# Optimization experiments

Hardware: AMD Instinct MI355X
Metric: run time of the kernel (lower is better)

## Reference

```python
import jax, jax.numpy as jnp
import numpy as np

EPS = 1e-8
TAU = 0.2
IOU_THR = 0.5
NEG = -1e9
N, C, H, D_FG, D_CLS = 8192, 1024, 256, 64, 128


def setup_inputs() -> dict:
    key = jax.random.key(0)
    ks = jax.random.split(key, 11)
    def lin(k, fan_in, fan_out):
        return jax.random.normal(k, (fan_in, fan_out), jnp.float32) / np.sqrt(fan_in)
    return {
        "roi_feats": jax.random.normal(ks[0], (N, C), jnp.float32),
        "labels": jax.random.randint(ks[1], (N,), 0, 21, jnp.int32).astype(jnp.int64),
        "ious": jax.random.uniform(ks[2], (N,), jnp.float32),
        "fg_w1": lin(ks[3], C, H), "fg_b1": jnp.zeros((H,), jnp.float32),
        "fg_w2": lin(ks[4], H, D_FG), "fg_b2": jnp.zeros((D_FG,), jnp.float32),
        "cls_w1": lin(ks[5], C, H), "cls_b1": jnp.zeros((H,), jnp.float32),
        "cls_w2": lin(ks[6], H, D_CLS), "cls_b2": jnp.zeros((D_CLS,), jnp.float32),
    }


def _project_normalize(x, w1, b1, w2, b2):
    h = jax.nn.relu(x @ w1 + b1)
    z = h @ w2 + b2
    norm = jnp.maximum(jnp.linalg.norm(z, axis=1, keepdims=True), EPS)
    return z / norm


def _forward(roi_feats, labels, ious, fg_w1, fg_b1, fg_w2, fg_b2, cls_w1, cls_b1, cls_w2, cls_b2):
    n = roi_feats.shape[0]
    z_fg = _project_normalize(roi_feats, fg_w1, fg_b1, fg_w2, fg_b2)
    z_cls = _project_normalize(roi_feats, cls_w1, cls_b1, cls_w2, cls_b2)

    ignore = labels == -1
    fg = (labels > 0) & ~ignore
    iou_weight = jnp.where(ious > IOU_THR, ious, 0.0)
    eye = jnp.eye(n, dtype=bool)

    # ---- fg/bg contrastive (bg_as_negatives_only=True) ----
    sim_fg = (z_fg @ z_fg.T) / TAU                       # [N,N]
    exp_sim = jnp.exp(sim_fg)
    denom = jnp.sum(exp_sim * (~eye).astype(jnp.float32), axis=1)
    pos = (fg & ~ignore)[None, :] & ~eye                 # positives: fg columns, no self
    n_pos = jnp.sum(pos, axis=1)
    numer = jnp.sum(exp_sim * pos.astype(jnp.float32), axis=1)
    # original computes den = denom + EPS then -log((numer+EPS)/(den+EPS))
    loss_i = -jnp.log((numer + EPS) / (denom + 2.0 * EPS))
    valid = (fg & ~ignore) & (n_pos > 0)
    w = iou_weight * valid.astype(jnp.float32)
    loss_fg_bg = jnp.sum(w * loss_i) / (jnp.sum(w) + EPS)

    # ---- class supervised contrastive ----
    sim_cls = (z_cls @ z_cls.T) / TAU
    sim_masked = jnp.where(eye, NEG, sim_cls)
    log_denom = jax.nn.logsumexp(sim_masked, axis=1)     # [N]
    log_p = jnp.where(eye, NEG, sim_cls - log_denom[:, None])
    # pos_mask keeps diagonal (as in original): same label, col not ignore, col label != 0
    posc = (labels[None, :] == labels[:, None]) & (~ignore)[None, :] & (labels[None, :] != 0)
    n_posc = jnp.sum(posc, axis=1).astype(jnp.float32)
    sum_log_p = jnp.sum(log_p * posc.astype(jnp.float32), axis=1)
    valid_c = (fg & ~ignore) & (n_posc > 0) & jnp.isfinite(log_denom)
    Lzi = jnp.where(valid_c, -sum_log_p / (n_posc + EPS), 0.0)
    wc = iou_weight * valid_c.astype(jnp.float32)
    loss_supcon = jnp.sum(wc * Lzi) / (jnp.sum(wc) + EPS)

    return jnp.stack([loss_fg_bg, loss_supcon])


def reference(roi_feats, labels, ious, fg_w1, fg_b1, fg_w2, fg_b2, cls_w1, cls_b1, cls_w2, cls_b2):
    return _forward(roi_feats, labels, ious, fg_w1, fg_b1, fg_w2, fg_b2, cls_w1, cls_b1, cls_w2, cls_b2)
```

## Files before the change

kernel.cpp:

```cpp
#include <hip/hip_runtime.h>


typedef __attribute__((ext_vector_type(8))) short bs8;
typedef __attribute__((ext_vector_type(4))) float f4;

#define MFMA_BF16(a, b, c) __builtin_amdgcn_mfma_f32_16x16x32_bf16((a), (b), (c), 0, 0, 0)

#if defined(__has_builtin)
#if __has_builtin(__builtin_amdgcn_exp2f)
#define EXP2F(x) __builtin_amdgcn_exp2f(x)
#endif
#endif
#ifndef EXP2F
__device__ __forceinline__ float __exp2_raw(float x) {
  float r;
  asm volatile("v_exp_f32 %0, %1" : "=v"(r) : "v"(x));
  return r;
}
#define EXP2F(x) __exp2_raw(x)
#endif

#define SQRT_KL2E 2.6857914f
#define LN2F      0.6931471805599453f

__device__ __forceinline__ unsigned short f2bf(float f) {
  unsigned int u = __float_as_uint(f);
  u = (u + 0x7fffu + ((u >> 16) & 1u)) >> 16;
  return (unsigned short)u;
}
__device__ __forceinline__ float bf2f(unsigned short s) {
  return __uint_as_float(((unsigned int)s) << 16);
}
__device__ __forceinline__ unsigned int pk_trunc(float a, float b) {
  return __builtin_amdgcn_perm(__float_as_uint(b), __float_as_uint(a), 0x07060302u);
}

constexpr size_t O_W1T  = 0;
constexpr size_t O_W2TF = 1048576;
constexpr size_t O_W2TC = 1081344;
constexpr size_t O_SCLS = 1146880;
constexpr size_t O_ROWD = 1163264;
constexpr size_t O_ROWN = 1196032;
constexpr size_t O_ROWS = 1228800;
constexpr size_t O_SCAL = 1261568;
constexpr size_t O_HIST = 1261584;
constexpr size_t O_NFG  = 1261712;
constexpr size_t O_H    = 1261824;
constexpr size_t O_ZF   = 9650432;
constexpr size_t O_ZC   = 10699008;
constexpr size_t O_XB   = 12796160;
constexpr size_t WS_NEED_XB = O_XB + 16777216;
constexpr int ZERO_WORDS = (int)((O_SCAL + 16 - O_SCLS) / 4);

__global__ void __launch_bounds__(256) prep_kernel(
    const float* __restrict__ X, const int* __restrict__ labels,
    const float* __restrict__ fgw1, const float* __restrict__ clsw1,
    const float* __restrict__ fgw2, const float* __restrict__ clsw2,
    unsigned short* __restrict__ W1T, unsigned short* __restrict__ W2Tf,
    unsigned short* __restrict__ W2Tc, float* __restrict__ zerop,
    int* __restrict__ hist, int* __restrict__ nfg,
    unsigned short* __restrict__ Xb) {
  const int bx = blockIdx.x, t = threadIdx.x;
  if (bx < 113) {
    int i = bx * 256 + t;
    if (i < ZERO_WORDS) zerop[i] = 0.f;
    return;
  }
  if (bx == 113) {
    __shared__ int sh[33];
    if (t < 33) sh[t] = 0;
    __syncthreads();
    for (int it = 0; it < 32; it++) {
      int lab = labels[it * 256 + t];
      if (lab >= 0 && lab < 32) atomicAdd(&sh[lab], 1);
      if (lab > 0) atomicAdd(&sh[32], 1);
    }
    __syncthreads();
    if (t < 32) hist[t] = sh[t];
    if (t == 32) *nfg = sh[32];
    return;
  }
  if (bx < 254) {
    __shared__ float tile[64][65];
    int lb = bx - 114;
    const float* src; unsigned short* dst; int R, C, lt;
    if (lb < 64)       { src = fgw1;  dst = W1T;              R = 1024; C = 256; lt = lb; }
    else if (lb < 128) { src = clsw1; dst = W1T + 256 * 1024; R = 1024; C = 256; lt = lb - 64; }
    else if (lb < 132) { src = fgw2;  dst = W2Tf;             R = 256;  C = 64;  lt = lb - 128; }
    else               { src = clsw2; dst = W2Tc;             R = 256;  C = 128; lt = lb - 132; }
    const int cT = C >> 6;
    const int r0 = (lt / cT) << 6, c0 = (lt % cT) << 6;
    {
      const int rr = t >> 4, cc = (t & 15) << 2;
#pragma unroll
      for (int i = 0; i < 4; i++) {
        float4 v = *(const float4*)(src + (size_t)(r0 + rr + i * 16) * C + c0 + cc);
        tile[rr + i * 16][cc] = v.x; tile[rr + i * 16][cc + 1] = v.y;
        tile[rr + i * 16][cc + 2] = v.z; tile[rr + i * 16][cc + 3] = v.w;
      }
    }
    __syncthreads();
    {
      const int dr = t >> 2, dc = (t & 3) << 4;
      bs8 o0, o1;
#pragma unroll
      for (int j = 0; j < 8; j++) o0[j] = (short)f2bf(tile[dc + j][dr]);
#pragma unroll
      for (int j = 0; j < 8; j++) o1[j] = (short)f2bf(tile[dc + 8 + j][dr]);
      unsigned short* dp = dst + (size_t)(c0 + dr) * R + r0 + dc;
      *(bs8*)dp = o0;
      *(bs8*)(dp + 8) = o1;
    }
    return;
  }
  {
    int i = (bx - 254) * 2048 + t * 8;
    float4 x0 = *(const float4*)(X + i);
    float4 x1 = *(const float4*)(X + i + 4);
    uint4 pk;
    pk.x = pk_trunc(x0.x, x0.y);
    pk.y = pk_trunc(x0.z, x0.w);
    pk.z = pk_trunc(x1.x, x1.y);
    pk.w = pk_trunc(x1.z, x1.w);
    *(uint4*)(Xb + i) = pk;
  }
}

__global__ void __launch_bounds__(256) gemm1x_kernel(
    const unsigned short* __restrict__ Xb, const unsigned short* __restrict__ W1T,
    const float* __restrict__ b1f, const float* __restrict__ b1c,
    unsigned short* __restrict__ H) {
  __shared__ __align__(16) unsigned short lA[128 * 72];
  __shared__ __align__(16) unsigned short lB[64 * 72];
  const int t = threadIdx.x;
  const int w = t >> 6, lane = t & 63, ln = lane & 15, quad = lane >> 4;
  const int m0 = blockIdx.x * 128, n0 = blockIdx.y * 64;

  f4 acc[2][4];
#pragma unroll
  for (int rs = 0; rs < 2; rs++)
#pragma unroll
    for (int s = 0; s < 4; s++) acc[rs][s] = (f4){0.f, 0.f, 0.f, 0.f};

  for (int k0 = 0; k0 < 1024; k0 += 64) {
    __syncthreads();
#pragma unroll
    for (int i = 0; i < 4; i++) {
      int c = i * 256 + t, r = c >> 3, ke = (c & 7) * 8;
      *(bs8*)&lA[r * 72 + ke] = *(const bs8*)(Xb + (size_t)(m0 + r) * 1024 + k0 + ke);
    }
#pragma unroll
    for (int i = 0; i < 2; i++) {
      int c = i * 256 + t, r = c >> 3, ke = (c & 7) * 8;
      *(bs8*)&lB[r * 72 + ke] = *(const bs8*)(W1T + (size_t)(n0 + r) * 1024 + k0 + ke);
    }
    __syncthreads();
#pragma unroll
    for (int kk = 0; kk < 2; kk++) {
      bs8 a0 = *(const bs8*)&lA[(w * 32 + ln) * 72 + kk * 32 + quad * 8];
      bs8 a1 = *(const bs8*)&lA[(w * 32 + 16 + ln) * 72 + kk * 32 + quad * 8];
#pragma unroll
      for (int s = 0; s < 4; s++) {
        bs8 bf = *(const bs8*)&lB[(s * 16 + ln) * 72 + kk * 32 + quad * 8];
        acc[0][s] = MFMA_BF16(a0, bf, acc[0][s]);
        acc[1][s] = MFMA_BF16(a1, bf, acc[1][s]);
      }
    }
  }
#pragma unroll
  for (int s = 0; s < 4; s++) {
    int n = n0 + s * 16 + ln;
    float b = (n < 256) ? b1f[n] : b1c[n - 256];
#pragma unroll
    for (int rs = 0; rs < 2; rs++)
#pragma unroll
      for (int r = 0; r < 4; r++) {
        float v = fmaxf(acc[rs][s][r] + b, 0.f);
        H[(size_t)(m0 + w * 32 + rs * 16 + quad * 4 + r) * 512 + n] = f2bf(v);
      }
  }
}

__global__ void __launch_bounds__(256) gemm1f_kernel(
    const float* __restrict__ X, const unsigned short* __restrict__ W1T,
    const float* __restrict__ b1f, const float* __restrict__ b1c,
    unsigned short* __restrict__ H) {
  __shared__ __align__(16) unsigned short lA[128 * 40];
  __shared__ __align__(16) unsigned short lB[64 * 40];
  const int t = threadIdx.x;
  const int w = t >> 6, lane = t & 63, ln = lane & 15, quad = lane >> 4;
  const int m0 = blockIdx.x * 128, n0 = blockIdx.y * 64;
  f4 acc[2][4];
#pragma unroll
  for (int rs = 0; rs < 2; rs++)
#pragma unroll
    for (int s = 0; s < 4; s++) acc[rs][s] = (f4){0.f, 0.f, 0.f, 0.f};
  for (int k0 = 0; k0 < 1024; k0 += 32) {
    __syncthreads();
#pragma unroll
    for (int i = 0; i < 2; i++) {
      int ch = t + i * 256;
      int r = ch >> 2, c = (ch & 3) * 8;
      const float* xp = X + (size_t)(m0 + r) * 1024 + k0 + c;
      float4 x0 = *(const float4*)xp;
      float4 x1 = *(const float4*)(xp + 4);
      uint4 pk;
      pk.x = pk_trunc(x0.x, x0.y); pk.y = pk_trunc(x0.z, x0.w);
      pk.z = pk_trunc(x1.x, x1.y); pk.w = pk_trunc(x1.z, x1.w);
      *(uint4*)&lA[r * 40 + c] = pk;
    }
    {
      int r = t >> 2, c = (t & 3) * 8;
      *(bs8*)&lB[r * 40 + c] = *(const bs8*)(W1T + (size_t)(n0 + r) * 1024 + k0 + c);
    }
    __syncthreads();
    bs8 af0 = *(const bs8*)&lA[(w * 32 + ln) * 40 + quad * 8];
    bs8 af1 = *(const bs8*)&lA[(w * 32 + 16 + ln) * 40 + quad * 8];
#pragma unroll
    for (int s = 0; s < 4; s++) {
      bs8 bf = *(const bs8*)&lB[(s * 16 + ln) * 40 + quad * 8];
      acc[0][s] = MFMA_BF16(af0, bf, acc[0][s]);
      acc[1][s] = MFMA_BF16(af1, bf, acc[1][s]);
    }
  }
#pragma unroll
  for (int s = 0; s < 4; s++) {
    int n = n0 + s * 16 + ln;
    float b = (n < 256) ? b1f[n] : b1c[n - 256];
#pragma unroll
    for (int rs = 0; rs < 2; rs++)
#pragma unroll
      for (int r = 0; r < 4; r++) {
        float v = fmaxf(acc[rs][s][r] + b, 0.f);
        H[(size_t)(m0 + w * 32 + rs * 16 + quad * 4 + r) * 512 + n] = f2bf(v);
      }
  }
}

__global__ void __launch_bounds__(256) gemm2_kernel(
    const unsigned short* __restrict__ H,
    const unsigned short* __restrict__ W2Tf, const unsigned short* __restrict__ W2Tc,
    const float* __restrict__ b2f, const float* __restrict__ b2c,
    unsigned short* __restrict__ Zf, unsigned short* __restrict__ Zc) {
  __shared__ float lredf[64][17];
  __shared__ float lredc[64][33];
  const int t = threadIdx.x;
  const int w = t >> 6, lane = t & 63, ln = lane & 15, quad = lane >> 4;
  const int rw = blockIdx.x * 16;
  const int kh = w & 1;

  if (w < 2) {
    const unsigned short* hrow = H + (size_t)(rw + ln) * 512 + kh * 128;
    f4 acc[4];
#pragma unroll
    for (int s = 0; s < 4; s++) acc[s] = (f4){0.f, 0.f, 0.f, 0.f};
#pragma unroll
    for (int ks = 0; ks < 4; ks++) {
      bs8 af = *(const bs8*)(hrow + ks * 32 + quad * 8);
#pragma unroll
      for (int s = 0; s < 4; s++) {
        bs8 bf = *(const bs8*)(W2Tf + (size_t)(s * 16 + ln) * 256 + kh * 128 + ks * 32 + quad * 8);
        acc[s] = MFMA_BF16(af, bf, acc[s]);
      }
    }
    if (kh) {
#pragma unroll
      for (int s = 0; s < 4; s++)
#pragma unroll
        for (int r = 0; r < 4; r++) lredf[lane][s * 4 + r] = acc[s][r];
    }
    __syncthreads();
    if (w == 0) {
      float ss[4] = {0.f, 0.f, 0.f, 0.f};
#pragma unroll
      for (int s = 0; s < 4; s++) {
        float b = b2f[s * 16 + ln];
#pragma unroll
        for (int r = 0; r < 4; r++) {
          acc[s][r] += lredf[lane][s * 4 + r] + b;
          ss[r] = fmaf(acc[s][r], acc[s][r], ss[r]);
        }
      }
#pragma unroll
      for (int r = 0; r < 4; r++) {
#pragma unroll
        for (int off = 1; off < 16; off <<= 1) ss[r] += __shfl_xor(ss[r], off, 64);
        float sc = SQRT_KL2E / fmaxf(sqrtf(ss[r]), 1e-8f);
#pragma unroll
        for (int s = 0; s < 4; s++)
          Zf[(size_t)(rw + quad * 4 + r) * 64 + s * 16 + ln] = f2bf(acc[s][r] * sc);
      }
    }
  } else {
    const unsigned short* hrow = H + (size_t)(rw + ln) * 512 + 256 + kh * 128;
    f4 acc[8];
#pragma unroll
    for (int s = 0; s < 8; s++) acc[s] = (f4){0.f, 0.f, 0.f, 0.f};
#pragma unroll
    for (int ks = 0; ks < 4; ks++) {
      bs8 af = *(const bs8*)(hrow + ks * 32 + quad * 8);
#pragma unroll
      for (int s = 0; s < 8; s++) {
        bs8 bf = *(const bs8*)(W2Tc + (size_t)(s * 16 + ln) * 256 + kh * 128 + ks * 32 + quad * 8);
        acc[s] = MFMA_BF16(af, bf, acc[s]);
      }
    }
    if (kh) {
#pragma unroll
      for (int s = 0; s < 8; s++)
#pragma unroll
        for (int r = 0; r < 4; r++) lredc[lane][s * 4 + r] = acc[s][r];
    }
    __syncthreads();
    if (w == 2) {
      float ss[4] = {0.f, 0.f, 0.f, 0.f};
#pragma unroll
      for (int s = 0; s < 8; s++) {
        float b = b2c[s * 16 + ln];
#pragma unroll
        for (int r = 0; r < 4; r++) {
          acc[s][r] += lredc[lane][s * 4 + r] + b;
          ss[r] = fmaf(acc[s][r], acc[s][r], ss[r]);
        }
      }
#pragma unroll
      for (int r = 0; r < 4; r++) {
#pragma unroll
        for (int off = 1; off < 16; off <<= 1) ss[r] += __shfl_xor(ss[r], off, 64);
        float sc = SQRT_KL2E / fmaxf(sqrtf(ss[r]), 1e-8f);
#pragma unroll
        for (int s = 0; s < 8; s++)
          Zc[(size_t)(rw + quad * 4 + r) * 128 + s * 16 + ln] = f2bf(acc[s][r] * sc);
      }
    }
  }
}

__global__ void __launch_bounds__(128) scls_kernel(const unsigned short* __restrict__ Zc,
                                                   const int* __restrict__ labels,
                                                   float* __restrict__ Scls) {
  const int c = blockIdx.x + 1;
  const int t = threadIdx.x;
  const int r0 = blockIdx.y * 128;
  float acc = 0.f;
#pragma unroll 4
  for (int r = r0; r < r0 + 128; r++) {
    if (labels[r] == c) acc += bf2f(Zc[(size_t)r * 128 + t]);
  }
  atomicAdd(&Scls[c * 128 + t], acc);
}

__global__ void __launch_bounds__(256, 3) sim_kernel(
    const unsigned short* __restrict__ Zf, const unsigned short* __restrict__ Zc,
    const int* __restrict__ labels,
    float* __restrict__ rowD, float* __restrict__ rowN, float* __restrict__ rowS) {
  __shared__ __align__(16) unsigned short sZf[128 * 68];
  __shared__ __align__(16) unsigned short sZc[128 * 132];
  __shared__ float sFg[128];
  const int t = threadIdx.x;
  const int w = t >> 6, lane = t & 63, ln = lane & 15, quad = lane >> 4;
  const int rbase = blockIdx.x * 128 + w * 32;

  bs8 afg[2][2], acl[2][4];
#pragma unroll
  for (int rs = 0; rs < 2; rs++) {
    const unsigned short* zf = Zf + (size_t)(rbase + rs * 16 + ln) * 64;
    const unsigned short* zc = Zc + (size_t)(rbase + rs * 16 + ln) * 128;
#pragma unroll
    for (int s = 0; s < 2; s++) afg[rs][s] = *(const bs8*)(zf + s * 32 + quad * 8);
#pragma unroll
    for (int s = 0; s < 4; s++) acl[rs][s] = *(const bs8*)(zc + s * 32 + quad * 8);
  }

  float dacc[2][4] = {}, nacc[2][4] = {}, sacc[2][4] = {};

  for (int ct = 0; ct < 4; ct++) {
    const int c0 = blockIdx.y * 512 + ct * 128;
    if (ct) __syncthreads();
#pragma unroll
    for (int i = 0; i < 4; i++) {
      int c = i * 256 + t, j = c >> 3, k8 = (c & 7) * 8;
      *(bs8*)&sZf[j * 68 + k8] = *(const bs8*)(Zf + (size_t)(c0 + j) * 64 + k8);
    }
#pragma unroll
    for (int i = 0; i < 8; i++) {
      int c = i * 256 + t, j = c >> 4, k8 = (c & 15) * 8;
      *(bs8*)&sZc[j * 132 + k8] = *(const bs8*)(Zc + (size_t)(c0 + j) * 128 + k8);
    }
    if (t < 128) sFg[t] = (labels[c0 + t] > 0) ? 1.f : 0.f;
    __syncthreads();

#pragma unroll 2
    for (int cg = 0; cg < 8; cg++) {
      const int lcol = cg * 16 + ln;
      const float fgc = sFg[lcol];
      bs8 b0 = *(const bs8*)&sZf[lcol * 68 + quad * 8];
      bs8 b1 = *(const bs8*)&sZf[lcol * 68 + 32 + quad * 8];
      bs8 bc0 = *(const bs8*)&sZc[lcol * 132 + quad * 8];
      bs8 bc1 = *(const bs8*)&sZc[lcol * 132 + 32 + quad * 8];
      bs8 bc2 = *(const bs8*)&sZc[lcol * 132 + 64 + quad * 8];
      bs8 bc3 = *(const bs8*)&sZc[lcol * 132 + 96 + quad * 8];
#pragma unroll
      for (int rs = 0; rs < 2; rs++) {
        f4 cf = {0.f, 0.f, 0.f, 0.f};
        cf = MFMA_BF16(afg[rs][0], b0, cf);
        cf = MFMA_BF16(afg[rs][1], b1, cf);
#pragma unroll
        for (int r = 0; r < 4; r++) {
          float e = EXP2F(cf[r]);
          dacc[rs][r] += e;
          nacc[rs][r] = fmaf(fgc, e, nacc[rs][r]);
        }
        f4 cs = {0.f, 0.f, 0.f, 0.f};
        cs = MFMA_BF16(acl[rs][0], bc0, cs);
        cs = MFMA_BF16(acl[rs][1], bc1, cs);
        cs = MFMA_BF16(acl[rs][2], bc2, cs);
        cs = MFMA_BF16(acl[rs][3], bc3, cs);
#pragma unroll
        for (int r = 0; r < 4; r++) sacc[rs][r] += EXP2F(cs[r]);
      }
    }
  }

#pragma unroll
  for (int rs = 0; rs < 2; rs++)
#pragma unroll
    for (int r = 0; r < 4; r++) {
      float d = dacc[rs][r], n = nacc[rs][r], s = sacc[rs][r];
#pragma unroll
      for (int off = 1; off < 16; off <<= 1) {
        d += __shfl_xor(d, off, 64);
        n += __shfl_xor(n, off, 64);
        s += __shfl_xor(s, off, 64);
      }
      if (ln == 0) {
        int row = rbase + rs * 16 + quad * 4 + r;
        atomicAdd(&rowD[row], d);
        atomicAdd(&rowN[row], n);
        atomicAdd(&rowS[row], s);
      }
    }
}

__global__ void __launch_bounds__(256) finalize_kernel(
    const unsigned short* __restrict__ Zf, const unsigned short* __restrict__ Zc,
    const int* __restrict__ labels, const float* __restrict__ ious,
    const float* __restrict__ rowD, const float* __restrict__ rowN,
    const float* __restrict__ rowS, const float* __restrict__ Scls,
    const int* __restrict__ hist, const int* __restrict__ nfg,
    float* __restrict__ scal) {
  __shared__ float red[4][4];
  const int t = threadIdx.x, w = t >> 6, lane = t & 63;
  float aw0 = 0.f, al0 = 0.f, aw1 = 0.f, al1 = 0.f;
  const int NFG = *nfg;
  for (int it = 0; it < 16; it++) {
    const int i = it * 512 + blockIdx.x * 4 + w;
    const int lab = labels[i];
    if (lab > 0 && lab < 32) {
      const float iou = ious[i];
      const float iw = (iou > 0.5f) ? iou : 0.f;
      float dot = 0.f, ssq = 0.f;
#pragma unroll
      for (int p = 0; p < 2; p++) {
        const int k = lane + p * 64;
        const float z = bf2f(Zc[(size_t)i * 128 + k]);
        dot = fmaf(z, Scls[lab * 128 + k], dot);
        ssq = fmaf(z, z, ssq);
      }
      float zf = bf2f(Zf[(size_t)i * 64 + lane]);
      float ssqf = zf * zf;
#pragma unroll
      for (int off = 1; off < 64; off <<= 1) {
        dot += __shfl_xor(dot, off, 64);
        ssq += __shfl_xor(ssq, off, 64);
        ssqf += __shfl_xor(ssqf, off, 64);
      }
      if (lane == 0) {
        const float ef = EXP2F(ssqf);
        if (NFG - 1 > 0) {
          const float D = rowD[i] - ef;
          const float Nn = rowN[i] - ef;
          const float loss = logf(D + 2e-8f) - logf(Nn + 1e-8f);
          aw0 += iw;
          al0 += iw * loss;
        }
        const int npc = hist[lab];
        if (npc > 0) {
          const float S = rowS[i] - EXP2F(ssq);
          const float logden = logf(S);
          const float slp = (dot - ssq) * LN2F - (float)(npc - 1) * logden - 1e9f;
          aw1 += iw;
          al1 += iw * (-slp / ((float)npc + 1e-8f));
        }
      }
    }
  }
  if (lane == 0) { red[w][0] = aw0; red[w][1] = al0; red[w][2] = aw1; red[w][3] = al1; }
  __syncthreads();
  if (t < 4) atomicAdd(&scal[t], red[0][t] + red[1][t] + red[2][t] + red[3][t]);
}

__global__ void writeout_kernel(const float* __restrict__ scal, float* __restrict__ out) {
  if (threadIdx.x == 0) {
    out[0] = scal[1] / (scal[0] + 1e-8f);
    out[1] = scal[3] / (scal[2] + 1e-8f);
  }
}

extern "C" void kernel_launch(void* const* d_in, const int* in_sizes, int n_in,
                              void* d_out, int out_size, void* d_ws, size_t ws_size,
                              hipStream_t stream) {
  (void)in_sizes; (void)n_in; (void)out_size;
  const float* roi    = (const float*)d_in[0];
  const int*   labels = (const int*)d_in[1];
  const float* ious   = (const float*)d_in[2];
  const float* fgw1   = (const float*)d_in[3];
  const float* fgb1   = (const float*)d_in[4];
  const float* fgw2   = (const float*)d_in[5];
  const float* fgb2   = (const float*)d_in[6];
  const float* clsw1  = (const float*)d_in[7];
  const float* clsb1  = (const float*)d_in[8];
  const float* clsw2  = (const float*)d_in[9];
  const float* clsb2  = (const float*)d_in[10];

  char* ws = (char*)d_ws;
  unsigned short* W1T  = (unsigned short*)(ws + O_W1T);
  unsigned short* W2Tf = (unsigned short*)(ws + O_W2TF);
  unsigned short* W2Tc = (unsigned short*)(ws + O_W2TC);
  unsigned short* Hb   = (unsigned short*)(ws + O_H);
  unsigned short* Zf   = (unsigned short*)(ws + O_ZF);
  unsigned short* Zc   = (unsigned short*)(ws + O_ZC);
  unsigned short* Xb   = (unsigned short*)(ws + O_XB);
  float* Scls = (float*)(ws + O_SCLS);
  float* rowD = (float*)(ws + O_ROWD);
  float* rowN = (float*)(ws + O_ROWN);
  float* rowS = (float*)(ws + O_ROWS);
  float* scal = (float*)(ws + O_SCAL);
  int* hist = (int*)(ws + O_HIST);
  int* nfg  = (int*)(ws + O_NFG);
  float* out = (float*)d_out;

  const bool useXb = ws_size >= WS_NEED_XB;
  const int prepBlocks = useXb ? 4350 : 254;

  hipLaunchKernelGGL(prep_kernel, dim3(prepBlocks), dim3(256), 0, stream,
                     roi, labels, fgw1, clsw1, fgw2, clsw2,
                     W1T, W2Tf, W2Tc, (float*)(ws + O_SCLS), hist, nfg, Xb);
  if (useXb) {
    hipLaunchKernelGGL(gemm1x_kernel, dim3(64, 8), dim3(256), 0, stream,
                       Xb, W1T, fgb1, clsb1, Hb);
  } else {
    hipLaunchKernelGGL(gemm1f_kernel, dim3(64, 8), dim3(256), 0, stream,
                       roi, W1T, fgb1, clsb1, Hb);
  }
  hipLaunchKernelGGL(gemm2_kernel, dim3(512), dim3(256), 0, stream,
                     Hb, W2Tf, W2Tc, fgb2, clsb2, Zf, Zc);
  hipLaunchKernelGGL(scls_kernel, dim3(20, 64), dim3(128), 0, stream, Zc, labels, Scls);
  hipLaunchKernelGGL(sim_kernel, dim3(64, 16), dim3(256), 0, stream,
                     Zf, Zc, labels, rowD, rowN, rowS);
  hipLaunchKernelGGL(finalize_kernel, dim3(128), dim3(256), 0, stream,
                     Zf, Zc, labels, ious, rowD, rowN, rowS, Scls, hist, nfg, scal);
  hipLaunchKernelGGL(writeout_kernel, dim3(1), dim3(64), 0, stream, scal, out);
}
```

Measured before the change: 222.4 us.

## Fuse class-sum kernel into sim kernel and enlarge per-warp row tile

Merges the per-class Zc summation into the similarity kernel as extra blocks, removing one launch. Each warp now covers 64 rows instead of 32, so every shared-memory column tile is reused across twice as many rows. Occupancy drops to 2 blocks per SIMD because the fragment and accumulator register arrays double. The finalize kernel is relaunched with more blocks and fewer iterations per block.

```diff
diff --git a/kernel.cpp b/kernel.cpp
--- a/kernel.cpp
+++ b/kernel.cpp
@@ -336,34 +336,36 @@
   }
 }
 
-__global__ void __launch_bounds__(128) scls_kernel(const unsigned short* __restrict__ Zc,
-                                                   const int* __restrict__ labels,
-                                                   float* __restrict__ Scls) {
-  const int c = blockIdx.x + 1;
-  const int t = threadIdx.x;
-  const int r0 = blockIdx.y * 128;
-  float acc = 0.f;
-#pragma unroll 4
-  for (int r = r0; r < r0 + 128; r++) {
-    if (labels[r] == c) acc += bf2f(Zc[(size_t)r * 128 + t]);
-  }
-  atomicAdd(&Scls[c * 128 + t], acc);
-}
-
-__global__ void __launch_bounds__(256, 3) sim_kernel(
+__global__ void __launch_bounds__(256, 2) simscls_kernel(
     const unsigned short* __restrict__ Zf, const unsigned short* __restrict__ Zc,
     const int* __restrict__ labels,
-    float* __restrict__ rowD, float* __restrict__ rowN, float* __restrict__ rowS) {
+    float* __restrict__ rowD, float* __restrict__ rowN, float* __restrict__ rowS,
+    float* __restrict__ Scls) {
+  const int bx = blockIdx.x;
+  const int t = threadIdx.x;
+  if (bx >= 512) {
+    const int b = bx - 512;
+    const int c = (b >> 6) + 1;
+    const int r0 = (b & 63) * 128 + (t >> 7) * 64;
+    const int col = t & 127;
+    float acc = 0.f;
+#pragma unroll 4
+    for (int r = r0; r < r0 + 64; r++) {
+      if (labels[r] == c) acc += bf2f(Zc[(size_t)r * 128 + col]);
+    }
+    atomicAdd(&Scls[c * 128 + col], acc);
+    return;
+  }
   __shared__ __align__(16) unsigned short sZf[128 * 68];
   __shared__ __align__(16) unsigned short sZc[128 * 132];
   __shared__ float sFg[128];
-  const int t = threadIdx.x;
   const int w = t >> 6, lane = t & 63, ln = lane & 15, quad = lane >> 4;
-  const int rbase = blockIdx.x * 128 + w * 32;
-
-  bs8 afg[2][2], acl[2][4];
-#pragma unroll
-  for (int rs = 0; rs < 2; rs++) {
+  const int rbase = (bx & 31) * 256 + w * 64;
+  const int ybase = (bx >> 5) * 512;
+
+  bs8 afg[4][2], acl[4][4];
+#pragma unroll
+  for (int rs = 0; rs < 4; rs++) {
     const unsigned short* zf = Zf + (size_t)(rbase + rs * 16 + ln) * 64;
     const unsigned short* zc = Zc + (size_t)(rbase + rs * 16 + ln) * 128;
 #pragma unroll
@@ -372,10 +374,10 @@
     for (int s = 0; s < 4; s++) acl[rs][s] = *(const bs8*)(zc + s * 32 + quad * 8);
   }
 
-  float dacc[2][4] = {}, nacc[2][4] = {}, sacc[2][4] = {};
+  float dacc[4][4] = {}, nacc[4][4] = {}, sacc[4][4] = {};
 
   for (int ct = 0; ct < 4; ct++) {
-    const int c0 = blockIdx.y * 512 + ct * 128;
+    const int c0 = ybase + ct * 128;
     if (ct) __syncthreads();
 #pragma unroll
     for (int i = 0; i < 4; i++) {
@@ -390,7 +392,6 @@
     if (t < 128) sFg[t] = (labels[c0 + t] > 0) ? 1.f : 0.f;
     __syncthreads();
 
-#pragma unroll 2
     for (int cg = 0; cg < 8; cg++) {
       const int lcol = cg * 16 + ln;
       const float fgc = sFg[lcol];
@@ -401,7 +402,7 @@
       bs8 bc2 = *(const bs8*)&sZc[lcol * 132 + 64 + quad * 8];
       bs8 bc3 = *(const bs8*)&sZc[lcol * 132 + 96 + quad * 8];
 #pragma unroll
-      for (int rs = 0; rs < 2; rs++) {
+      for (int rs = 0; rs < 4; rs++) {
         f4 cf = {0.f, 0.f, 0.f, 0.f};
         cf = MFMA_BF16(afg[rs][0], b0, cf);
         cf = MFMA_BF16(afg[rs][1], b1, cf);
@@ -423,7 +424,7 @@
   }
 
 #pragma unroll
-  for (int rs = 0; rs < 2; rs++)
+  for (int rs = 0; rs < 4; rs++)
 #pragma unroll
     for (int r = 0; r < 4; r++) {
       float d = dacc[rs][r], n = nacc[rs][r], s = sacc[rs][r];
@@ -453,8 +454,8 @@
   const int t = threadIdx.x, w = t >> 6, lane = t & 63;
   float aw0 = 0.f, al0 = 0.f, aw1 = 0.f, al1 = 0.f;
   const int NFG = *nfg;
-  for (int it = 0; it < 16; it++) {
-    const int i = it * 512 + blockIdx.x * 4 + w;
+  for (int it = 0; it < 4; it++) {
+    const int i = it * 2048 + blockIdx.x * 4 + w;
     const int lab = labels[i];
     if (lab > 0 && lab < 32) {
       const float iou = ious[i];
@@ -555,10 +556,9 @@
   }
   hipLaunchKernelGGL(gemm2_kernel, dim3(512), dim3(256), 0, stream,
                      Hb, W2Tf, W2Tc, fgb2, clsb2, Zf, Zc);
-  hipLaunchKernelGGL(scls_kernel, dim3(20, 64), dim3(128), 0, stream, Zc, labels, Scls);
-  hipLaunchKernelGGL(sim_kernel, dim3(64, 16), dim3(256), 0, stream,
-                     Zf, Zc, labels, rowD, rowN, rowS);
-  hipLaunchKernelGGL(finalize_kernel, dim3(128), dim3(256), 0, stream,
+  hipLaunchKernelGGL(simscls_kernel, dim3(1792), dim3(256), 0, stream,
+                     Zf, Zc, labels, rowD, rowN, rowS, Scls);
+  hipLaunchKernelGGL(finalize_kernel, dim3(512), dim3(256), 0, stream,
                      Zf, Zc, labels, ious, rowD, rowN, rowS, Scls, hist, nfg, scal);
   hipLaunchKernelGGL(writeout_kernel, dim3(1), dim3(64), 0, stream, scal, out);
 }
```

Measured after the change: 375.0 us. 68.6% more time.
